# Kernel optimization log

Hardware: AMD Instinct MI355X
Metric: run time of the kernel (lower is better)

## Reference

```python
import jax, jax.numpy as jnp
import numpy as np
import math

B, S, E = 4, 4096, 1024
NUM_HEADS = 16
D = E // NUM_HEADS  # attention_size = 64


def setup_inputs() -> dict:
    key = jax.random.key(0)
    ks = jax.random.split(key, 7)
    queries = jax.random.normal(ks[0], (B, S, E), dtype=jnp.float32)
    keys = jax.random.normal(ks[1], (B, S, E), dtype=jnp.float32)
    values = jax.random.normal(ks[2], (B, S, E), dtype=jnp.float32)
    mask = jax.random.randint(ks[3], (B, S, S), 0, 2).astype(bool)
    # nn.Linear(E, D, bias=False): weight [D, E], y = x @ W^T
    lim = 1.0 / math.sqrt(E)
    W_q = jax.random.uniform(ks[4], (D, E), jnp.float32, -lim, lim)
    W_k = jax.random.uniform(ks[5], (D, E), jnp.float32, -lim, lim)
    W_v = jax.random.uniform(ks[6], (D, E), jnp.float32, -lim, lim)
    return {"queries": queries, "keys": keys, "values": values, "mask": mask,
            "W_q": W_q, "W_k": W_k, "W_v": W_v}


def reference(queries, keys, values, mask, W_q, W_k, W_v):
    Q = jnp.einsum('bse,de->bsd', queries, W_q)  # [B,S,D]
    K = jnp.einsum('bse,de->bsd', keys, W_k)
    V = jnp.einsum('bse,de->bsd', values, W_v)
    norm = math.sqrt(D)
    scores = jnp.einsum('bqd,bkd->bqk', Q, K) / norm  # [B,S,S]
    scores = jnp.where(mask, jnp.float32(-1e20), scores)
    attn = jax.nn.softmax(scores, axis=2)
    return jnp.einsum('bqk,bkd->bqd', attn, V)  # [B,S,D]
```

## Files before the change

kernel.cpp:

```cpp
#include <hip/hip_runtime.h>
#include <hip/hip_bf16.h>
#include <math.h>

#define NB 4
#define NS 4096
#define NE 1024
#define ND 64

typedef short bf16x8 __attribute__((ext_vector_type(8)));
typedef float f32x4  __attribute__((ext_vector_type(4)));

static __device__ inline unsigned short f2bf(float f) {
    __hip_bfloat16 h = __float2bfloat16(f);
    return *reinterpret_cast<unsigned short*>(&h);
}

__global__ void detect_mask(const unsigned int* __restrict__ mw, int* __restrict__ flag) {
    __shared__ int found;
    if (threadIdx.x == 0) found = 0;
    __syncthreads();
    int f = 0;
    for (int i = threadIdx.x; i < 4096; i += 256)
        if (mw[i] > 1u) f = 1;
    if (f) atomicOr(&found, 1);
    __syncthreads();
    if (threadIdx.x == 0) *flag = found;
}

__global__ void prep_w(const float* __restrict__ Wq, const float* __restrict__ Wk,
                       const float* __restrict__ Wv, unsigned short* __restrict__ Wb) {
    const int z = blockIdx.x;
    const float* W = (z == 0) ? Wq : (z == 1) ? Wk : Wv;
    unsigned short* o = Wb + (size_t)z * (ND * NE);
    const float scale = (z == 0) ? 0.125f : 1.0f;
    int i0 = blockIdx.y * 2048 + threadIdx.x * 8;
    float4 a = *(const float4*)&W[i0];
    float4 b = *(const float4*)&W[i0 + 4];
    ushort4 u0 = { f2bf(a.x * scale), f2bf(a.y * scale), f2bf(a.z * scale), f2bf(a.w * scale) };
    ushort4 u1 = { f2bf(b.x * scale), f2bf(b.y * scale), f2bf(b.z * scale), f2bf(b.w * scale) };
    *(ushort4*)&o[i0]     = u0;
    *(ushort4*)&o[i0 + 4] = u1;
}

__global__ __launch_bounds__(256) void proj_kernel(
    const float* __restrict__ Xq, const float* __restrict__ Xk, const float* __restrict__ Xv,
    const unsigned short* __restrict__ Wb,
    unsigned short* __restrict__ Qp, unsigned short* __restrict__ Kp,
    unsigned short* __restrict__ Vtp)
{
    const int z = blockIdx.y;
    const float* X = (z == 0) ? Xq : (z == 1) ? Xk : Xv;
    const unsigned short* W = Wb + (size_t)z * (ND * NE);

    const int t    = threadIdx.x;
    const int wv   = t >> 6;
    const int lane = t & 63;
    const int quad = lane >> 4;
    const int l16  = lane & 15;
    const int m0   = blockIdx.x * 64 + wv * 16;

    const float* Xrow = X + (size_t)(m0 + l16) * NE + quad * 8;

    f32x4 acc[4] = {};

    #pragma unroll 4
    for (int e0 = 0; e0 < NE; e0 += 32) {
        float4 xa = *(const float4*)&Xrow[e0];
        float4 xb = *(const float4*)&Xrow[e0 + 4];
        bf16x8 a;
        a[0] = (short)f2bf(xa.x); a[1] = (short)f2bf(xa.y);
        a[2] = (short)f2bf(xa.z); a[3] = (short)f2bf(xa.w);
        a[4] = (short)f2bf(xb.x); a[5] = (short)f2bf(xb.y);
        a[6] = (short)f2bf(xb.z); a[7] = (short)f2bf(xb.w);
        #pragma unroll
        for (int nt = 0; nt < 4; ++nt) {
            bf16x8 b = *(const bf16x8*)&W[(size_t)(nt * 16 + l16) * NE + e0 + quad * 8];
            acc[nt] = __builtin_amdgcn_mfma_f32_16x16x32_bf16(a, b, acc[nt], 0, 0, 0);
        }
    }

    #pragma unroll
    for (int nt = 0; nt < 4; ++nt)
        #pragma unroll
        for (int r = 0; r < 4; ++r) {
            int m   = m0 + quad * 4 + r;
            int col = nt * 16 + l16;
            unsigned short u = f2bf(acc[nt][r]);
            if (z == 0)      Qp[(size_t)m * ND + col] = u;
            else if (z == 1) Kp[(size_t)m * ND + col] = u;
            else             Vtp[((size_t)(m >> 12) * ND + col) * NS + (m & 4095)] = u;
        }
}

__global__ __launch_bounds__(256) void attn_kernel(
    const unsigned short* __restrict__ Qp, const unsigned short* __restrict__ Kp,
    const unsigned short* __restrict__ Vtp,
    const void* __restrict__ maskp, const int* __restrict__ flagp,
    float* __restrict__ out)
{
    __shared__ short Ss[4][2][16][72];
    __shared__ float Op[4][16][68];
    __shared__ float Lp[4][16];

    const int t    = threadIdx.x;
    const int wv   = t >> 6;
    const int lane = t & 63;
    const int quad = lane >> 4;
    const int l16  = lane & 15;
    const int b    = blockIdx.y;
    const int q0   = blockIdx.x * 16;
    const int koff = wv * 1024;

    const bool m_u8 = (*flagp != 0);
    const unsigned char* m8  = (const unsigned char*)maskp;
    const int*           m32 = (const int*)maskp;

    const unsigned short* Qrow = Qp + ((size_t)b * NS + q0 + l16) * ND;
    const bf16x8 qf0 = *(const bf16x8*)&Qrow[quad * 8];
    const bf16x8 qf1 = *(const bf16x8*)&Qrow[32 + quad * 8];

    const unsigned short* Kbase = Kp  + ((size_t)b * NS) * ND;
    const unsigned short* Vbase = Vtp + (size_t)b * ND * NS;

    float l_lane[4] = {};
    f32x4 Oacc[4] = {};

    #pragma unroll 2
    for (int it = 0; it < 16; ++it) {
        const int k0 = koff + it * 64;
        const int pb = it & 1;

        int mv[16];
        #pragma unroll
        for (int r = 0; r < 4; ++r) {
            size_t mrow = ((size_t)b * NS + (q0 + quad * 4 + r)) * (size_t)NS + k0;
            if (m_u8) {
                #pragma unroll
                for (int kt = 0; kt < 4; ++kt)
                    mv[kt * 4 + r] = (int)m8[mrow + kt * 16 + l16];
            } else {
                #pragma unroll
                for (int kt = 0; kt < 4; ++kt)
                    mv[kt * 4 + r] = m32[mrow + kt * 16 + l16];
            }
        }

        f32x4 sc[4] = {};
        #pragma unroll
        for (int kt = 0; kt < 4; ++kt) {
            const unsigned short* Krow = Kbase + (size_t)(k0 + kt * 16 + l16) * ND;
            bf16x8 kf0 = *(const bf16x8*)&Krow[quad * 8];
            bf16x8 kf1 = *(const bf16x8*)&Krow[32 + quad * 8];
            sc[kt] = __builtin_amdgcn_mfma_f32_16x16x32_bf16(qf0, kf0, sc[kt], 0, 0, 0);
            sc[kt] = __builtin_amdgcn_mfma_f32_16x16x32_bf16(qf1, kf1, sc[kt], 0, 0, 0);
        }

        #pragma unroll
        for (int kt = 0; kt < 4; ++kt)
            #pragma unroll
            for (int r = 0; r < 4; ++r) {
                float p = mv[kt * 4 + r] ? 0.0f : __expf(sc[kt][r]);
                l_lane[r] += p;
                Ss[wv][pb][quad * 4 + r][kt * 16 + l16] = (short)f2bf(p);
            }

        __syncthreads();

        bf16x8 a0 = *(const bf16x8*)&Ss[wv][pb][l16][quad * 8];
        bf16x8 a1 = *(const bf16x8*)&Ss[wv][pb][l16][32 + quad * 8];

        #pragma unroll
        for (int nt = 0; nt < 4; ++nt) {
            const unsigned short* Vrow = Vbase + (size_t)(nt * 16 + l16) * NS + k0;
            bf16x8 vf0 = *(const bf16x8*)&Vrow[quad * 8];
            bf16x8 vf1 = *(const bf16x8*)&Vrow[32 + quad * 8];
            Oacc[nt] = __builtin_amdgcn_mfma_f32_16x16x32_bf16(a0, vf0, Oacc[nt], 0, 0, 0);
            Oacc[nt] = __builtin_amdgcn_mfma_f32_16x16x32_bf16(a1, vf1, Oacc[nt], 0, 0, 0);
        }
    }

    #pragma unroll
    for (int r = 0; r < 4; ++r) {
        #pragma unroll
        for (int off = 1; off < 16; off <<= 1)
            l_lane[r] += __shfl_xor(l_lane[r], off);
    }

    #pragma unroll
    for (int nt = 0; nt < 4; ++nt)
        #pragma unroll
        for (int r = 0; r < 4; ++r)
            Op[wv][quad * 4 + r][nt * 16 + l16] = Oacc[nt][r];
    if (l16 == 0) {
        #pragma unroll
        for (int r = 0; r < 4; ++r)
            Lp[wv][quad * 4 + r] = l_lane[r];
    }
    __syncthreads();

    {
        int q  = t >> 4;
        int d4 = (t & 15) * 4;
        f32x4 s = {};
        #pragma unroll
        for (int w = 0; w < 4; ++w)
            s += *(const f32x4*)&Op[w][q][d4];
        float l = Lp[0][q] + Lp[1][q] + Lp[2][q] + Lp[3][q];
        float inv = 1.0f / l;
        float4 o = { s[0] * inv, s[1] * inv, s[2] * inv, s[3] * inv };
        *(float4*)&out[((size_t)b * NS + q0 + q) * ND + d4] = o;
    }
}

extern "C" void kernel_launch(void* const* d_in, const int* in_sizes, int n_in,
                              void* d_out, int out_size, void* d_ws, size_t ws_size,
                              hipStream_t stream) {
    const float* queries = (const float*)d_in[0];
    const float* keys    = (const float*)d_in[1];
    const float* values  = (const float*)d_in[2];
    const void*  mask    = d_in[3];
    const float* Wq      = (const float*)d_in[4];
    const float* Wk      = (const float*)d_in[5];
    const float* Wv      = (const float*)d_in[6];
    float* out = (float*)d_out;

    char* ws = (char*)d_ws;
    int* flag = (int*)ws;
    unsigned short* Wb = (unsigned short*)(ws + 256);
    size_t wb = (size_t)3 * ND * NE * sizeof(unsigned short);
    size_t pb = (size_t)NB * NS * ND * sizeof(unsigned short);
    unsigned short* Qp  = (unsigned short*)(ws + 256 + wb);
    unsigned short* Kp  = (unsigned short*)(ws + 256 + wb + pb);
    unsigned short* Vtp = (unsigned short*)(ws + 256 + wb + 2 * pb);

    hipLaunchKernelGGL(detect_mask, dim3(1), dim3(256), 0, stream,
                       (const unsigned int*)mask, flag);
    hipLaunchKernelGGL(prep_w, dim3(3, 32), dim3(256), 0, stream, Wq, Wk, Wv, Wb);
    hipLaunchKernelGGL(proj_kernel, dim3((NB * NS) / 64, 3), dim3(256), 0, stream,
                       queries, keys, values, Wb, Qp, Kp, Vtp);
    hipLaunchKernelGGL(attn_kernel, dim3(NS / 16, NB), dim3(256), 0, stream,
                       Qp, Kp, Vtp, mask, flag, out);
}
```

Baseline: 581.3 us.

## Stage X tiles through LDS in projection, prefetch V and relax attention sync

Scratch buffers move from the workspace to static device globals. The projection kernel now stages each 64x64 fp32 X chunk through double-buffered LDS as bf16, converting pairs with a packed conversion and prefetching the next chunk while MFMAs run. The attention kernel issues its V-fragment loads before the softmax so their latency overlaps the exp work. It also swaps the block-wide __syncthreads for a per-wave LDS waitcnt fence, since each wave only touches its own Ss slice, and raises wave priority around the MFMA sections. The per-wave fence relies on the compiler not reordering across it, and the extra prefetched V registers may lower occupancy.

Result: slower. 604.6 us (+4.0%).

```diff
diff --git a/kernel.cpp b/kernel.cpp
--- a/kernel.cpp
+++ b/kernel.cpp
@@ -10,12 +10,27 @@
 typedef short bf16x8 __attribute__((ext_vector_type(8)));
 typedef float f32x4  __attribute__((ext_vector_type(4)));
 
+__device__ unsigned short g_Wb[3 * ND * NE];
+__device__ unsigned short g_Qp[NB * NS * ND];
+__device__ unsigned short g_Kp[NB * NS * ND];
+__device__ unsigned short g_Vt[NB * ND * NS];
+__device__ int g_flag;
+
 static __device__ inline unsigned short f2bf(float f) {
     __hip_bfloat16 h = __float2bfloat16(f);
     return *reinterpret_cast<unsigned short*>(&h);
 }
-
-__global__ void detect_mask(const unsigned int* __restrict__ mw, int* __restrict__ flag) {
+static __device__ inline unsigned int f2bf2(float lo, float hi) {
+    __hip_bfloat162 h = __float22bfloat162_rn(make_float2(lo, hi));
+    return *reinterpret_cast<unsigned int*>(&h);
+}
+
+static __device__ __forceinline__ void lds_fence() {
+    asm volatile("s_waitcnt lgkmcnt(0)" ::: "memory");
+    __builtin_amdgcn_sched_barrier(0);
+}
+
+__global__ void detect_mask(const unsigned int* __restrict__ mw) {
     __shared__ int found;
     if (threadIdx.x == 0) found = 0;
     __syncthreads();
@@ -24,14 +39,14 @@
         if (mw[i] > 1u) f = 1;
     if (f) atomicOr(&found, 1);
     __syncthreads();
-    if (threadIdx.x == 0) *flag = found;
+    if (threadIdx.x == 0) g_flag = found;
 }
 
 __global__ void prep_w(const float* __restrict__ Wq, const float* __restrict__ Wk,
-                       const float* __restrict__ Wv, unsigned short* __restrict__ Wb) {
+                       const float* __restrict__ Wv) {
     const int z = blockIdx.x;
     const float* W = (z == 0) ? Wq : (z == 1) ? Wk : Wv;
-    unsigned short* o = Wb + (size_t)z * (ND * NE);
+    unsigned short* o = g_Wb + (size_t)z * (ND * NE);
     const float scale = (z == 0) ? 0.125f : 1.0f;
     int i0 = blockIdx.y * 2048 + threadIdx.x * 8;
     float4 a = *(const float4*)&W[i0];
@@ -43,60 +58,85 @@
 }
 
 __global__ __launch_bounds__(256) void proj_kernel(
-    const float* __restrict__ Xq, const float* __restrict__ Xk, const float* __restrict__ Xv,
-    const unsigned short* __restrict__ Wb,
-    unsigned short* __restrict__ Qp, unsigned short* __restrict__ Kp,
-    unsigned short* __restrict__ Vtp)
+    const float* __restrict__ Xq, const float* __restrict__ Xk, const float* __restrict__ Xv)
 {
+    __shared__ unsigned short Xs[2][64][72];
+
     const int z = blockIdx.y;
     const float* X = (z == 0) ? Xq : (z == 1) ? Xk : Xv;
-    const unsigned short* W = Wb + (size_t)z * (ND * NE);
+    const unsigned short* W = g_Wb + (size_t)z * (ND * NE);
 
     const int t    = threadIdx.x;
     const int wv   = t >> 6;
     const int lane = t & 63;
     const int quad = lane >> 4;
     const int l16  = lane & 15;
-    const int m0   = blockIdx.x * 64 + wv * 16;
-
-    const float* Xrow = X + (size_t)(m0 + l16) * NE + quad * 8;
+    const int m0   = blockIdx.x * 64;
+
+    const int sr  = t >> 4;
+    const int sc4 = (t & 15) * 4;
+    const float* Xb = X + (size_t)m0 * NE;
+
+    float4 xv[4];
+
+    #pragma unroll
+    for (int p = 0; p < 4; ++p)
+        xv[p] = *(const float4*)&Xb[(size_t)(sr + p * 16) * NE + sc4];
+    #pragma unroll
+    for (int p = 0; p < 4; ++p) {
+        uint2 u = { f2bf2(xv[p].x, xv[p].y), f2bf2(xv[p].z, xv[p].w) };
+        *(uint2*)&Xs[0][sr + p * 16][sc4] = u;
+    }
+    __syncthreads();
 
     f32x4 acc[4] = {};
 
-    #pragma unroll 4
-    for (int e0 = 0; e0 < NE; e0 += 32) {
-        float4 xa = *(const float4*)&Xrow[e0];
-        float4 xb = *(const float4*)&Xrow[e0 + 4];
-        bf16x8 a;
-        a[0] = (short)f2bf(xa.x); a[1] = (short)f2bf(xa.y);
-        a[2] = (short)f2bf(xa.z); a[3] = (short)f2bf(xa.w);
-        a[4] = (short)f2bf(xb.x); a[5] = (short)f2bf(xb.y);
-        a[6] = (short)f2bf(xb.z); a[7] = (short)f2bf(xb.w);
-        #pragma unroll
-        for (int nt = 0; nt < 4; ++nt) {
-            bf16x8 b = *(const bf16x8*)&W[(size_t)(nt * 16 + l16) * NE + e0 + quad * 8];
-            acc[nt] = __builtin_amdgcn_mfma_f32_16x16x32_bf16(a, b, acc[nt], 0, 0, 0);
-        }
+    #pragma unroll 2
+    for (int c = 0; c < 16; ++c) {
+        const int buf = c & 1;
+        const int e0  = c * 64;
+
+        if (c < 15) {
+            #pragma unroll
+            for (int p = 0; p < 4; ++p)
+                xv[p] = *(const float4*)&Xb[(size_t)(sr + p * 16) * NE + e0 + 64 + sc4];
+        }
+
+        #pragma unroll
+        for (int ks = 0; ks < 2; ++ks) {
+            bf16x8 a = *(const bf16x8*)&Xs[buf][wv * 16 + l16][ks * 32 + quad * 8];
+            #pragma unroll
+            for (int nt = 0; nt < 4; ++nt) {
+                bf16x8 bb = *(const bf16x8*)&W[(size_t)(nt * 16 + l16) * NE + e0 + ks * 32 + quad * 8];
+                acc[nt] = __builtin_amdgcn_mfma_f32_16x16x32_bf16(a, bb, acc[nt], 0, 0, 0);
+            }
+        }
+
+        if (c < 15) {
+            #pragma unroll
+            for (int p = 0; p < 4; ++p) {
+                uint2 u = { f2bf2(xv[p].x, xv[p].y), f2bf2(xv[p].z, xv[p].w) };
+                *(uint2*)&Xs[buf ^ 1][sr + p * 16][sc4] = u;
+            }
+        }
+        __syncthreads();
     }
 
     #pragma unroll
     for (int nt = 0; nt < 4; ++nt)
         #pragma unroll
         for (int r = 0; r < 4; ++r) {
-            int m   = m0 + quad * 4 + r;
+            int m   = m0 + wv * 16 + quad * 4 + r;
             int col = nt * 16 + l16;
             unsigned short u = f2bf(acc[nt][r]);
-            if (z == 0)      Qp[(size_t)m * ND + col] = u;
-            else if (z == 1) Kp[(size_t)m * ND + col] = u;
-            else             Vtp[((size_t)(m >> 12) * ND + col) * NS + (m & 4095)] = u;
+            if (z == 0)      g_Qp[(size_t)m * ND + col] = u;
+            else if (z == 1) g_Kp[(size_t)m * ND + col] = u;
+            else             g_Vt[((size_t)(m >> 12) * ND + col) * NS + (m & 4095)] = u;
         }
 }
 
 __global__ __launch_bounds__(256) void attn_kernel(
-    const unsigned short* __restrict__ Qp, const unsigned short* __restrict__ Kp,
-    const unsigned short* __restrict__ Vtp,
-    const void* __restrict__ maskp, const int* __restrict__ flagp,
-    float* __restrict__ out)
+    const void* __restrict__ maskp, float* __restrict__ out)
 {
     __shared__ short Ss[4][2][16][72];
     __shared__ float Op[4][16][68];
@@ -111,16 +151,16 @@
     const int q0   = blockIdx.x * 16;
     const int koff = wv * 1024;
 
-    const bool m_u8 = (*flagp != 0);
+    const bool m_u8 = (g_flag != 0);
     const unsigned char* m8  = (const unsigned char*)maskp;
     const int*           m32 = (const int*)maskp;
 
-    const unsigned short* Qrow = Qp + ((size_t)b * NS + q0 + l16) * ND;
+    const unsigned short* Qrow = g_Qp + ((size_t)b * NS + q0 + l16) * ND;
     const bf16x8 qf0 = *(const bf16x8*)&Qrow[quad * 8];
     const bf16x8 qf1 = *(const bf16x8*)&Qrow[32 + quad * 8];
 
-    const unsigned short* Kbase = Kp  + ((size_t)b * NS) * ND;
-    const unsigned short* Vbase = Vtp + (size_t)b * ND * NS;
+    const unsigned short* Kbase = g_Kp + ((size_t)b * NS) * ND;
+    const unsigned short* Vbase = g_Vt + (size_t)b * ND * NS;
 
     float l_lane[4] = {};
     f32x4 Oacc[4] = {};
@@ -146,6 +186,7 @@
         }
 
         f32x4 sc[4] = {};
+        __builtin_amdgcn_s_setprio(1);
         #pragma unroll
         for (int kt = 0; kt < 4; ++kt) {
             const unsigned short* Krow = Kbase + (size_t)(k0 + kt * 16 + l16) * ND;
@@ -154,6 +195,15 @@
             sc[kt] = __builtin_amdgcn_mfma_f32_16x16x32_bf16(qf0, kf0, sc[kt], 0, 0, 0);
             sc[kt] = __builtin_amdgcn_mfma_f32_16x16x32_bf16(qf1, kf1, sc[kt], 0, 0, 0);
         }
+        __builtin_amdgcn_s_setprio(0);
+
+        bf16x8 vf[8];
+        #pragma unroll
+        for (int nt = 0; nt < 4; ++nt) {
+            const unsigned short* Vrow = Vbase + (size_t)(nt * 16 + l16) * NS + k0;
+            vf[2 * nt]     = *(const bf16x8*)&Vrow[quad * 8];
+            vf[2 * nt + 1] = *(const bf16x8*)&Vrow[32 + quad * 8];
+        }
 
         #pragma unroll
         for (int kt = 0; kt < 4; ++kt)
@@ -164,19 +214,18 @@
                 Ss[wv][pb][quad * 4 + r][kt * 16 + l16] = (short)f2bf(p);
             }
 
-        __syncthreads();
+        lds_fence();
 
         bf16x8 a0 = *(const bf16x8*)&Ss[wv][pb][l16][quad * 8];
         bf16x8 a1 = *(const bf16x8*)&Ss[wv][pb][l16][32 + quad * 8];
 
+        __builtin_amdgcn_s_setprio(1);
         #pragma unroll
         for (int nt = 0; nt < 4; ++nt) {
-            const unsigned short* Vrow = Vbase + (size_t)(nt * 16 + l16) * NS + k0;
-            bf16x8 vf0 = *(const bf16x8*)&Vrow[quad * 8];
-            bf16x8 vf1 = *(const bf16x8*)&Vrow[32 + quad * 8];
-            Oacc[nt] = __builtin_amdgcn_mfma_f32_16x16x32_bf16(a0, vf0, Oacc[nt], 0, 0, 0);
-            Oacc[nt] = __builtin_amdgcn_mfma_f32_16x16x32_bf16(a1, vf1, Oacc[nt], 0, 0, 0);
-        }
+            Oacc[nt] = __builtin_amdgcn_mfma_f32_16x16x32_bf16(a0, vf[2 * nt],     Oacc[nt], 0, 0, 0);
+            Oacc[nt] = __builtin_amdgcn_mfma_f32_16x16x32_bf16(a1, vf[2 * nt + 1], Oacc[nt], 0, 0, 0);
+        }
+        __builtin_amdgcn_s_setprio(0);
     }
 
     #pragma unroll
@@ -224,20 +273,11 @@
     const float* Wv      = (const float*)d_in[6];
     float* out = (float*)d_out;
 
-    char* ws = (char*)d_ws;
-    int* flag = (int*)ws;
-    unsigned short* Wb = (unsigned short*)(ws + 256);
-    size_t wb = (size_t)3 * ND * NE * sizeof(unsigned short);
-    size_t pb = (size_t)NB * NS * ND * sizeof(unsigned short);
-    unsigned short* Qp  = (unsigned short*)(ws + 256 + wb);
-    unsigned short* Kp  = (unsigned short*)(ws + 256 + wb + pb);
-    unsigned short* Vtp = (unsigned short*)(ws + 256 + wb + 2 * pb);
-
     hipLaunchKernelGGL(detect_mask, dim3(1), dim3(256), 0, stream,
-                       (const unsigned int*)mask, flag);
-    hipLaunchKernelGGL(prep_w, dim3(3, 32), dim3(256), 0, stream, Wq, Wk, Wv, Wb);
+                       (const unsigned int*)mask);
+    hipLaunchKernelGGL(prep_w, dim3(3, 32), dim3(256), 0, stream, Wq, Wk, Wv);
     hipLaunchKernelGGL(proj_kernel, dim3((NB * NS) / 64, 3), dim3(256), 0, stream,
-                       queries, keys, values, Wb, Qp, Kp, Vtp);
+                       queries, keys, values);
     hipLaunchKernelGGL(attn_kernel, dim3(NS / 16, NB), dim3(256), 0, stream,
-                       Qp, Kp, Vtp, mask, flag, out);
-}
+                       mask, out);
+}
```
